# Optimization experiments

Hardware: AMD Instinct MI355X
Metric: run time of the kernel (lower is better)

## Reference

```python
import jax, jax.numpy as jnp
import numpy as np
from jax import lax

D_MODEL = 768
N_LAYER = 4
VOCAB = 50280  # 50277 padded to multiple of 8
D_INNER = 2 * D_MODEL
D_STATE = 16
D_CONV = 4
DT_RANK = 48  # ceil(768/16)
EPS = 1e-5


def setup_inputs() -> dict:
    key = jax.random.key(0)
    ks = iter(jax.random.split(key, 16))
    s = 0.02
    B, L = 1, 1024
    inp = {
        "input_ids": jax.random.randint(next(ks), (B, L), 0, 50277, dtype=jnp.int64).astype(jnp.int32),
        "embedding": jax.random.normal(next(ks), (VOCAB, D_MODEL), jnp.float32) * s,
        "in_proj_w": jax.random.normal(next(ks), (N_LAYER, 2 * D_INNER, D_MODEL), jnp.float32) * s,
        "conv_w": jax.random.normal(next(ks), (N_LAYER, D_INNER, 1, D_CONV), jnp.float32) * s,
        "conv_b": jnp.zeros((N_LAYER, D_INNER), jnp.float32),
        "x_proj_w": jax.random.normal(next(ks), (N_LAYER, DT_RANK + 2 * D_STATE, D_INNER), jnp.float32) * s,
        "dt_proj_w": jax.random.normal(next(ks), (N_LAYER, D_INNER, DT_RANK), jnp.float32) * s,
        "dt_proj_b": jax.random.uniform(next(ks), (N_LAYER, D_INNER), jnp.float32, -4.0, -2.0),
        "A_log": jnp.log(jnp.broadcast_to(jnp.arange(1, D_STATE + 1, dtype=jnp.float32), (N_LAYER, D_INNER, D_STATE))),
        "D_param": jnp.ones((N_LAYER, D_INNER), jnp.float32),
        "out_proj_w": jax.random.normal(next(ks), (N_LAYER, D_MODEL, D_INNER), jnp.float32) * s,
        "norm_w": jnp.ones((N_LAYER, D_MODEL), jnp.float32),
        "norm_f_w": jnp.ones((D_MODEL,), jnp.float32),
    }
    return inp


def rmsnorm(x, w):
    var = jnp.mean(jnp.square(x), axis=-1, keepdims=True)
    return x * lax.rsqrt(var + EPS) * w


def silu(x):
    return x * jax.nn.sigmoid(x)


def mamba_mixer(h, in_w, cw, cb, xw, dtw, dtb, A_log, Dp, ow):
    B, L, _ = h.shape
    xz = jnp.einsum("bld,ed->ble", h, in_w)          # [B,L,2*d_inner]
    x, z = jnp.split(xz, 2, axis=-1)
    # causal depthwise conv1d over length
    xc = lax.conv_general_dilated(
        x.transpose(0, 2, 1), cw, (1,), [(D_CONV - 1, 0)],
        dimension_numbers=("NCH", "OIH", "NCH"), feature_group_count=D_INNER,
    ).transpose(0, 2, 1) + cb                          # [B,L,d_inner]
    xc = silu(xc)
    dbl = jnp.einsum("bld,ed->ble", xc, xw)            # [B,L,R+2N]
    dt = jax.nn.softplus(jnp.einsum("blr,dr->bld", dbl[..., :DT_RANK], dtw) + dtb)
    Bm = dbl[..., DT_RANK:DT_RANK + D_STATE]           # [B,L,N]
    Cm = dbl[..., DT_RANK + D_STATE:]                  # [B,L,N]
    A = -jnp.exp(A_log)                                # [d_inner,N]
    dA = jnp.exp(dt[..., None] * A)                    # [B,L,d_inner,N]
    dBx = dt[..., None] * Bm[:, :, None, :] * xc[..., None]

    def step(s, inp):
        a, b, c = inp
        s = a * s + b
        y = jnp.einsum("bdn,bn->bd", s, c)
        return s, y

    s0 = jnp.zeros((B, D_INNER, D_STATE), h.dtype)
    _, ys = lax.scan(step, s0, (dA.transpose(1, 0, 2, 3), dBx.transpose(1, 0, 2, 3), Cm.transpose(1, 0, 2)))
    y = ys.transpose(1, 0, 2) + xc * Dp                # [B,L,d_inner]
    y = y * silu(z)
    return jnp.einsum("ble,de->bld", y, ow)


def reference(input_ids, embedding, in_proj_w, conv_w, conv_b, x_proj_w,
              dt_proj_w, dt_proj_b, A_log, D_param, out_proj_w, norm_w, norm_f_w):
    h = embedding[input_ids]                           # [B,L,D]
    for i in range(N_LAYER):
        h = h + mamba_mixer(rmsnorm(h, norm_w[i]), in_proj_w[i], conv_w[i], conv_b[i],
                            x_proj_w[i], dt_proj_w[i], dt_proj_b[i], A_log[i],
                            D_param[i], out_proj_w[i])
    h = rmsnorm(h, norm_f_w)
    logits = jnp.einsum("bld,vd->blv", h, embedding)   # tied lm_head
    return logits
```

## Files before the change

kernel.cpp:

```cpp
#include <hip/hip_runtime.h>
#include <cstdint>
#include <cstddef>

#define N_LAYER 4
#define VOCABSZ 50280
#define VOCABPAD 50304
#define DMODEL 768
#define DINNER 1536
#define DSTATE 16
#define DTRANK 48
#define SEQL 1024
#define HPSTRIDE (SEQL * DMODEL)

typedef __bf16 bf16x8 __attribute__((ext_vector_type(8)));
typedef unsigned short us8 __attribute__((ext_vector_type(8)));
typedef float f32x4 __attribute__((ext_vector_type(4)));

__device__ __forceinline__ unsigned short f2bf(float f) {
    unsigned int u = __builtin_bit_cast(unsigned int, f);
    u = (u + 0x7FFFu + ((u >> 16) & 1u)) >> 16;
    return (unsigned short)u;
}

__device__ __forceinline__ void glds16(const unsigned short* g, unsigned short* l) {
    __builtin_amdgcn_global_load_lds(
        (const __attribute__((address_space(1))) void*)g,
        (__attribute__((address_space(3))) void*)l, 16, 0, 0);
}

__device__ __forceinline__ void cvt8(const float* s, unsigned short* d) {
    const float4* s4 = (const float4*)s;
    float4 a = s4[0], b = s4[1];
    us8 o = { f2bf(a.x), f2bf(a.y), f2bf(a.z), f2bf(a.w),
              f2bf(b.x), f2bf(b.y), f2bf(b.z), f2bf(b.w) };
    *(us8*)d = o;
}

__global__ __launch_bounds__(256) void cvt_bf16_kernel(
    const float* __restrict__ src, unsigned short* __restrict__ dst, int n8)
{
    int i = blockIdx.x * 256 + threadIdx.x;
    if (i >= n8) return;
    cvt8(src + (size_t)i * 8, dst + (size_t)i * 8);
}

__global__ __launch_bounds__(256) void cvt3_kernel(
    const float* __restrict__ s0, unsigned short* __restrict__ d0, int n0,
    const float* __restrict__ s1, unsigned short* __restrict__ d1, int n1,
    const float* __restrict__ s2, unsigned short* __restrict__ d2, int n2)
{
    int i = blockIdx.x * 256 + threadIdx.x;
    const float* s; unsigned short* d; int j = i;
    if (j < n0) { s = s0; d = d0; }
    else {
        j -= n0;
        if (j < n1) { s = s1; d = d1; }
        else {
            j -= n1;
            if (j >= n2) return;
            s = s2; d = d2;
        }
    }
    cvt8(s + (size_t)j * 8, d + (size_t)j * 8);
}

__global__ __launch_bounds__(256) void cvt_xw_kernel(
    const float* __restrict__ xw, unsigned short* __restrict__ xwB)
{
    int g = blockIdx.x * 256 + threadIdx.x;
    if (g >= N_LAYER * 128 * 192) return;
    int row = g / 192;
    int c8  = g % 192;
    int layer = row >> 7;
    int r = row & 127;
    us8 o;
    if (r < 80) {
        const float4* s = (const float4*)(xw + ((size_t)(layer * 80 + r) * DINNER) + c8 * 8);
        float4 a = s[0], b = s[1];
        o = (us8){ f2bf(a.x), f2bf(a.y), f2bf(a.z), f2bf(a.w),
                   f2bf(b.x), f2bf(b.y), f2bf(b.z), f2bf(b.w) };
    } else {
        o = (us8){0, 0, 0, 0, 0, 0, 0, 0};
    }
    *(us8*)(xwB + (size_t)row * DINNER + c8 * 8) = o;
}

__device__ __forceinline__ void gemm_compute32(
    const unsigned short* sAbuf, const unsigned short* sBbuf,
    int wm, int wn, int frs, f32x4 (&acc)[4][4])
{
    bf16x8 af[4], bfr[4];
#pragma unroll
    for (int t = 0; t < 4; ++t) {
        af[t]  = __builtin_bit_cast(bf16x8, *(const us8*)&sAbuf[(wm + t * 16) * 32 + frs]);
        bfr[t] = __builtin_bit_cast(bf16x8, *(const us8*)&sBbuf[(wn + t * 16) * 32 + frs]);
    }
#pragma unroll
    for (int mt = 0; mt < 4; ++mt)
#pragma unroll
        for (int nt = 0; nt < 4; ++nt)
            acc[mt][nt] = __builtin_amdgcn_mfma_f32_16x16x32_bf16(
                af[mt], bfr[nt], acc[mt][nt], 0, 0, 0);
}

__device__ __forceinline__ void gemm_core(
    const unsigned short* __restrict__ A, const unsigned short* __restrict__ B,
    float* __restrict__ C, int N, int Kstride, int Klen, int bm, int bn)
{
    __shared__ unsigned short sA0[128 * 32];
    __shared__ unsigned short sA1[128 * 32];
    __shared__ unsigned short sB0[128 * 32];
    __shared__ unsigned short sB1[128 * 32];

    const int tid  = threadIdx.x;
    const int lane = tid & 63;
    const int wave = tid >> 6;
    const int wm = (wave & 1) * 64;
    const int wn = (wave >> 1) * 64;

    const int scol = ((tid & 3) ^ ((tid >> 3) & 3)) * 8;
    const unsigned short* Ag0 = A + (size_t)(bm + (tid >> 2)) * Kstride + scol;
    const unsigned short* Ag1 = Ag0 + (size_t)64 * Kstride;
    const unsigned short* Bg0 = B + (size_t)(bn + (tid >> 2)) * Kstride + scol;
    const unsigned short* Bg1 = Bg0 + (size_t)64 * Kstride;
    unsigned short* lA0a = sA0 + tid * 8;  unsigned short* lA0b = lA0a + 2048;
    unsigned short* lA1a = sA1 + tid * 8;  unsigned short* lA1b = lA1a + 2048;
    unsigned short* lB0a = sB0 + tid * 8;  unsigned short* lB0b = lB0a + 2048;
    unsigned short* lB1a = sB1 + tid * 8;  unsigned short* lB1b = lB1a + 2048;

    f32x4 acc[4][4];
#pragma unroll
    for (int i = 0; i < 4; ++i)
#pragma unroll
        for (int j = 0; j < 4; ++j) acc[i][j] = (f32x4){0.f, 0.f, 0.f, 0.f};

    const int frs = (lane & 15) * 32 + (((lane >> 4) ^ ((lane >> 1) & 3))) * 8;

    glds16(Ag0, lA0a); glds16(Ag1, lA0b);
    glds16(Bg0, lB0a); glds16(Bg1, lB0b);
    Ag0 += 32; Ag1 += 32; Bg0 += 32; Bg1 += 32;
    __syncthreads();

    for (int k0 = 0; k0 < Klen; k0 += 64) {
        glds16(Ag0, lA1a); glds16(Ag1, lA1b);
        glds16(Bg0, lB1a); glds16(Bg1, lB1b);
        Ag0 += 32; Ag1 += 32; Bg0 += 32; Bg1 += 32;
        gemm_compute32(sA0, sB0, wm, wn, frs, acc);
        __syncthreads();

        if (k0 + 64 < Klen) {
            glds16(Ag0, lA0a); glds16(Ag1, lA0b);
            glds16(Bg0, lB0a); glds16(Bg1, lB0b);
            Ag0 += 32; Ag1 += 32; Bg0 += 32; Bg1 += 32;
        }
        gemm_compute32(sA1, sB1, wm, wn, frs, acc);
        __syncthreads();
    }

    const int cn = lane & 15;
    const int cm = (lane >> 4) * 4;
#pragma unroll
    for (int mt = 0; mt < 4; ++mt) {
#pragma unroll
        for (int nt = 0; nt < 4; ++nt) {
            int n = bn + wn + nt * 16 + cn;
            if (n < N) {
#pragma unroll
                for (int r = 0; r < 4; ++r) {
                    int m = bm + wm + mt * 16 + cm + r;
                    C[(size_t)m * N + n] = acc[mt][nt][r];
                }
            }
        }
    }
}

__device__ __forceinline__ void swz_mn(int bid, int grid, int& bm, int& bn)
{
    int cpx = grid >> 3;
    int swz = (bid & 7) * cpx + (bid >> 3);
    bm = (swz & 7) << 7;
    bn = (swz >> 3) << 7;
}

__global__ __launch_bounds__(256) void gemm_in_kernel(
    const unsigned short* __restrict__ A, const unsigned short* __restrict__ B,
    float* __restrict__ C, int N, int K)
{ int bm, bn; swz_mn(blockIdx.x, gridDim.x, bm, bn); gemm_core(A, B, C, N, K, K, bm, bn); }

__global__ __launch_bounds__(256) void gemm_xproj_kernel(
    const unsigned short* __restrict__ A, const unsigned short* __restrict__ B,
    float* __restrict__ C, int N, int K)
{ int bm, bn; swz_mn(blockIdx.x, gridDim.x, bm, bn); gemm_core(A, B, C, N, K, K, bm, bn); }

__global__ __launch_bounds__(256) void gemm_logits_kernel(
    const unsigned short* __restrict__ A, const unsigned short* __restrict__ B,
    float* __restrict__ C, int N, int K)
{ int bm, bn; swz_mn(blockIdx.x, gridDim.x, bm, bn); gemm_core(A, B, C, N, K, K, bm, bn); }

__global__ __launch_bounds__(256) void gemm_outp_kernel(
    const unsigned short* __restrict__ A, const unsigned short* __restrict__ B,
    float* __restrict__ hp, int N, int Kstride, int Klen)
{
    int bid = blockIdx.x;
    int split = bid / 48;
    int r = bid - split * 48;
    int swz = (r & 7) * 6 + (r >> 3);
    int bm = (swz & 7) << 7;
    int bn = (swz >> 3) << 7;
    int kbase = split * Klen;
    gemm_core(A + kbase, B + kbase, hp + (size_t)split * HPSTRIDE,
              N, Kstride, Klen, bm, bn);
}

template <int ADD>
__global__ __launch_bounds__(256) void gemm_fb_kernel(
    const float* __restrict__ A, const float* __restrict__ B,
    const float* __restrict__ ADDSRC, float* __restrict__ C,
    int N, int K)
{
    __shared__ unsigned short sA[128 * 40];
    __shared__ unsigned short sB[128 * 40];
    const int tid  = threadIdx.x;
    const int lane = tid & 63;
    const int wave = tid >> 6;
    const int wm = (wave & 1) * 64;
    const int wn = (wave >> 1) * 64;
    const int bm = blockIdx.y * 128;
    const int bn = blockIdx.x * 128;
    const int srow = tid >> 1;
    const int scol = (tid & 1) * 16;
    const float* Ap = A + (size_t)(bm + srow) * K + scol;
    const int brow  = bn + srow;
    const bool bvalid = brow < N;
    const float* Bp = B + (size_t)(bvalid ? brow : 0) * K + scol;
    f32x4 acc[4][4];
#pragma unroll
    for (int i = 0; i < 4; ++i)
#pragma unroll
        for (int j = 0; j < 4; ++j) acc[i][j] = (f32x4){0.f, 0.f, 0.f, 0.f};
    unsigned short* sAp = &sA[srow * 40 + scol];
    unsigned short* sBp = &sB[srow * 40 + scol];
    const int fr = (lane & 15) * 40 + (lane >> 4) * 8;
    for (int k0 = 0; k0 < K; k0 += 32) {
        float4 a0 = *(const float4*)(Ap + k0);
        float4 a1 = *(const float4*)(Ap + k0 + 4);
        float4 a2 = *(const float4*)(Ap + k0 + 8);
        float4 a3 = *(const float4*)(Ap + k0 + 12);
        float4 b0, b1, b2, b3;
        if (bvalid) {
            b0 = *(const float4*)(Bp + k0);
            b1 = *(const float4*)(Bp + k0 + 4);
            b2 = *(const float4*)(Bp + k0 + 8);
            b3 = *(const float4*)(Bp + k0 + 12);
        } else {
            b0 = make_float4(0.f, 0.f, 0.f, 0.f);
            b1 = b0; b2 = b0; b3 = b0;
        }
        __syncthreads();
        us8 va0 = { f2bf(a0.x), f2bf(a0.y), f2bf(a0.z), f2bf(a0.w),
                    f2bf(a1.x), f2bf(a1.y), f2bf(a1.z), f2bf(a1.w) };
        us8 va1 = { f2bf(a2.x), f2bf(a2.y), f2bf(a2.z), f2bf(a2.w),
                    f2bf(a3.x), f2bf(a3.y), f2bf(a3.z), f2bf(a3.w) };
        us8 vb0 = { f2bf(b0.x), f2bf(b0.y), f2bf(b0.z), f2bf(b0.w),
                    f2bf(b1.x), f2bf(b1.y), f2bf(b1.z), f2bf(b1.w) };
        us8 vb1 = { f2bf(b2.x), f2bf(b2.y), f2bf(b2.z), f2bf(b2.w),
                    f2bf(b3.x), f2bf(b3.y), f2bf(b3.z), f2bf(b3.w) };
        *(us8*)(sAp)     = va0;
        *(us8*)(sAp + 8) = va1;
        *(us8*)(sBp)     = vb0;
        *(us8*)(sBp + 8) = vb1;
        __syncthreads();
        bf16x8 af[4], bfr[4];
#pragma unroll
        for (int t = 0; t < 4; ++t) {
            af[t]  = __builtin_bit_cast(bf16x8, *(const us8*)&sA[wm * 40 + t * 640 + fr]);
            bfr[t] = __builtin_bit_cast(bf16x8, *(const us8*)&sB[wn * 40 + t * 640 + fr]);
        }
#pragma unroll
        for (int mt = 0; mt < 4; ++mt)
#pragma unroll
            for (int nt = 0; nt < 4; ++nt)
                acc[mt][nt] = __builtin_amdgcn_mfma_f32_16x16x32_bf16(
                    af[mt], bfr[nt], acc[mt][nt], 0, 0, 0);
    }
    const int cn = lane & 15;
    const int cm = (lane >> 4) * 4;
#pragma unroll
    for (int mt = 0; mt < 4; ++mt) {
#pragma unroll
        for (int nt = 0; nt < 4; ++nt) {
            int n = bn + wn + nt * 16 + cn;
            if (n < N) {
#pragma unroll
                for (int r = 0; r < 4; ++r) {
                    int m = bm + wm + mt * 16 + cm + r;
                    size_t idx = (size_t)m * N + n;
                    float v = acc[mt][nt][r];
                    if constexpr (ADD) v += ADDSRC[idx];
                    C[idx] = v;
                }
            }
        }
    }
}

__global__ __launch_bounds__(256) void embed_kernel(
    const int* __restrict__ ids, const float* __restrict__ emb, float* __restrict__ h)
{
    int l = blockIdx.x;
    int id = ids[l];
    const float* src = emb + (size_t)id * DMODEL;
    for (int d = threadIdx.x; d < DMODEL; d += 256) h[(size_t)l * DMODEL + d] = src[d];
}

template <typename OT>
__global__ __launch_bounds__(256) void rmsnorm_kernel(
    const float* __restrict__ x, const float* __restrict__ w,
    OT* __restrict__ out, int D)
{
    int l = blockIdx.x;
    const float* xr = x + (size_t)l * D;
    float ss = 0.f;
    for (int d = threadIdx.x; d < D; d += 256) { float v = xr[d]; ss += v * v; }
#pragma unroll
    for (int off = 32; off > 0; off >>= 1) ss += __shfl_down(ss, off, 64);
    __shared__ float red[4];
    __shared__ float invs;
    if ((threadIdx.x & 63) == 0) red[threadIdx.x >> 6] = ss;
    __syncthreads();
    if (threadIdx.x == 0)
        invs = rsqrtf((red[0] + red[1] + red[2] + red[3]) / (float)D + 1e-5f);
    __syncthreads();
    float inv = invs;
    for (int d = threadIdx.x; d < D; d += 256) {
        float v = xr[d] * inv * w[d];
        if constexpr (sizeof(OT) == 2) out[(size_t)l * D + d] = f2bf(v);
        else                           out[(size_t)l * D + d] = v;
    }
}

__global__ __launch_bounds__(256) void rmsnorm_acc_kernel(
    float* __restrict__ h, const float* __restrict__ hp,
    const float* __restrict__ w, unsigned short* __restrict__ out)
{
    int l = blockIdx.x;
    const size_t base = (size_t)l * DMODEL;
    __shared__ float row[DMODEL];
    float ss = 0.f;
    for (int d = threadIdx.x; d < DMODEL; d += 256) {
        float v = h[base + d]
                + hp[base + d]
                + hp[base + d + (size_t)HPSTRIDE]
                + hp[base + d + (size_t)2 * HPSTRIDE]
                + hp[base + d + (size_t)3 * HPSTRIDE];
        row[d] = v;
        h[base + d] = v;
        ss += v * v;
    }
#pragma unroll
    for (int off = 32; off > 0; off >>= 1) ss += __shfl_down(ss, off, 64);
    __shared__ float red[4];
    __shared__ float invs;
    if ((threadIdx.x & 63) == 0) red[threadIdx.x >> 6] = ss;
    __syncthreads();
    if (threadIdx.x == 0)
        invs = rsqrtf((red[0] + red[1] + red[2] + red[3]) / (float)DMODEL + 1e-5f);
    __syncthreads();
    float inv = invs;
    for (int d = threadIdx.x; d < DMODEL; d += 256)
        out[base + d] = f2bf(row[d] * inv * w[d]);
}

__global__ __launch_bounds__(256) void conv_silu_kernel(
    const float* __restrict__ xz, const float* __restrict__ cw,
    const float* __restrict__ cb, float* __restrict__ xc,
    unsigned short* __restrict__ xcB)
{
    int l = blockIdx.x / 6;
    int d = (blockIdx.x % 6) * 256 + threadIdx.x;
    float w0 = cw[d * 4], w1 = cw[d * 4 + 1], w2 = cw[d * 4 + 2], w3 = cw[d * 4 + 3];
    float acc = cb[d];
    if (l >= 3) acc += xz[(size_t)(l - 3) * 3072 + d] * w0;
    if (l >= 2) acc += xz[(size_t)(l - 2) * 3072 + d] * w1;
    if (l >= 1) acc += xz[(size_t)(l - 1) * 3072 + d] * w2;
    acc += xz[(size_t)l * 3072 + d] * w3;
    float sig = 1.f / (1.f + __expf(-acc));
    float v = acc * sig;
    size_t idx = (size_t)l * DINNER + d;
    xc[idx]  = v;
    xcB[idx] = f2bf(v);
}

__global__ __launch_bounds__(256) void xproj_kernel(
    const float* __restrict__ xc, const float* __restrict__ xw, float* __restrict__ dbl)
{
    int l = blockIdx.x;
    __shared__ float sx[DINNER];
    for (int d = threadIdx.x; d < DINNER; d += 256) sx[d] = xc[(size_t)l * DINNER + d];
    __syncthreads();
    int wave = threadIdx.x >> 6, lane = threadIdx.x & 63;
    for (int e = wave * 20; e < wave * 20 + 20; ++e) {
        const float* wr = xw + (size_t)e * DINNER;
        float s = 0.f;
        for (int d = lane; d < DINNER; d += 64) s += sx[d] * wr[d];
#pragma unroll
        for (int off = 32; off > 0; off >>= 1) s += __shfl_down(s, off, 64);
        if (lane == 0) dbl[l * 80 + e] = s;
    }
}

__global__ __launch_bounds__(256) void dtproj_kernel(
    const float* __restrict__ dbl, const float* __restrict__ dtw,
    const float* __restrict__ dtb, float* __restrict__ dt)
{
    int l = blockIdx.x / 6;
    int e = (blockIdx.x % 6) * 256 + threadIdx.x;
    __shared__ float sd[48];
    if (threadIdx.x < 48) sd[threadIdx.x] = dbl[l * 80 + threadIdx.x];
    __syncthreads();
    float a = dtb[e];
    const float4* wr = (const float4*)(dtw + (size_t)e * 48);
#pragma unroll
    for (int q = 0; q < 12; ++q) {
        float4 w4 = wr[q];
        a += sd[q * 4] * w4.x + sd[q * 4 + 1] * w4.y + sd[q * 4 + 2] * w4.z + sd[q * 4 + 3] * w4.w;
    }
    dt[(size_t)l * DINNER + e] = (a > 20.f) ? a : log1pf(__expf(a));
}

template <typename OT>
__global__ __launch_bounds__(64) void scan_kernel(
    const float* __restrict__ dt, const float* __restrict__ dbl,
    const float* __restrict__ xc, const float* __restrict__ xz,
    const float* __restrict__ alog, const float* __restrict__ dpar,
    OT* __restrict__ yf)
{
    int d0 = blockIdx.x * 4;
    int lane = threadIdx.x;
    int n = lane & 15;
    int dloc = lane >> 4;
    int d = d0 + dloc;
    float A = -__expf(alog[d * 16 + n]);
    float Dq[4];
#pragma unroll
    for (int q = 0; q < 4; ++q) Dq[q] = dpar[d0 + q];

    __shared__ float sdt[64][4];
    __shared__ float sxc[64][4];
    __shared__ float sz[64][4];
    __shared__ float sB[64][16];
    __shared__ float sC[64][16];
    __shared__ float pp[4][64][17];

    float s = 0.f;
    for (int c0 = 0; c0 < SEQL; c0 += 64) {
        int l = c0 + lane;
        *(float4*)&sdt[lane][0] = *(const float4*)&dt[(size_t)l * DINNER + d0];
        *(float4*)&sxc[lane][0] = *(const float4*)&xc[(size_t)l * DINNER + d0];
        *(float4*)&sz[lane][0]  = *(const float4*)&xz[(size_t)l * 3072 + DINNER + d0];
#pragma unroll
        for (int q = 0; q < 4; ++q) {
            *(float4*)&sB[lane][q * 4] = *(const float4*)&dbl[l * 80 + 48 + q * 4];
            *(float4*)&sC[lane][q * 4] = *(const float4*)&dbl[l * 80 + 64 + q * 4];
        }
        __syncthreads();
#pragma unroll 4
        for (int j = 0; j < 64; ++j) {
            float dtv = sdt[j][dloc];
            float xv  = sxc[j][dloc];
            float a = __expf(dtv * A);
            s = fmaf(a, s, dtv * sB[j][n] * xv);
            pp[dloc][j][n] = s * sC[j][n];
        }
        __syncthreads();
#pragma unroll
        for (int q = 0; q < 4; ++q) {
            float accv = 0.f;
#pragma unroll
            for (int nn = 0; nn < 16; ++nn) accv += pp[q][lane][nn];
            float xv = sxc[lane][q];
            float zv = sz[lane][q];
            float sig = 1.f / (1.f + __expf(-zv));
            float v = (accv + xv * Dq[q]) * (zv * sig);
            if constexpr (sizeof(OT) == 2) yf[(size_t)(c0 + lane) * DINNER + d0 + q] = f2bf(v);
            else                           yf[(size_t)(c0 + lane) * DINNER + d0 + q] = v;
        }
        __syncthreads();
    }
}

__global__ __launch_bounds__(64) void scan_fused_kernel(
    const float* __restrict__ dbl, const float* __restrict__ xc,
    const float* __restrict__ xz, const float* __restrict__ dtw,
    const float* __restrict__ dtb, const float* __restrict__ alog,
    const float* __restrict__ dpar, unsigned short* __restrict__ yf)
{
    int d0 = blockIdx.x * 4;
    int lane = threadIdx.x;
    int n = lane & 15;
    int dloc = lane >> 4;
    int d = d0 + dloc;
    float A = -__expf(alog[d * 16 + n]);
    float Dq[4], dtbq[4];
#pragma unroll
    for (int q = 0; q < 4; ++q) { Dq[q] = dpar[d0 + q]; dtbq[q] = dtb[d0 + q]; }

    __shared__ float swt[4][48];
    for (int t = lane; t < 192; t += 64)
        swt[t / 48][t % 48] = dtw[(size_t)(d0 + t / 48) * 48 + t % 48];

    __shared__ float sdt[64][4];
    __shared__ float sxc[64][4];
    __shared__ float sz[64][4];
    __shared__ float sB[64][16];
    __shared__ float sC[64][16];
    __shared__ float pp[4][64][17];
    __syncthreads();

    float s = 0.f;
    for (int c0 = 0; c0 < SEQL; c0 += 64) {
        int l = c0 + lane;
        *(float4*)&sxc[lane][0] = *(const float4*)&xc[(size_t)l * DINNER + d0];
        *(float4*)&sz[lane][0]  = *(const float4*)&xz[(size_t)l * 3072 + DINNER + d0];
        float4 db[12];
#pragma unroll
        for (int q4 = 0; q4 < 12; ++q4)
            db[q4] = *(const float4*)&dbl[l * 80 + q4 * 4];
#pragma unroll
        for (int q = 0; q < 4; ++q) {
            *(float4*)&sB[lane][q * 4] = *(const float4*)&dbl[l * 80 + 48 + q * 4];
            *(float4*)&sC[lane][q * 4] = *(const float4*)&dbl[l * 80 + 64 + q * 4];
        }
#pragma unroll
        for (int q = 0; q < 4; ++q) {
            float a = dtbq[q];
#pragma unroll
            for (int q4 = 0; q4 < 12; ++q4) {
                float4 w4 = *(const float4*)&swt[q][q4 * 4];
                a += db[q4].x * w4.x + db[q4].y * w4.y + db[q4].z * w4.z + db[q4].w * w4.w;
            }
            sdt[lane][q] = (a > 20.f) ? a : log1pf(__expf(a));
        }
        __syncthreads();
#pragma unroll 4
        for (int j = 0; j < 64; ++j) {
            float dtv = sdt[j][dloc];
            float xv  = sxc[j][dloc];
            float a = __expf(dtv * A);
            s = fmaf(a, s, dtv * sB[j][n] * xv);
            pp[dloc][j][n] = s * sC[j][n];
        }
        __syncthreads();
#pragma unroll
        for (int q = 0; q < 4; ++q) {
            float accv = 0.f;
#pragma unroll
            for (int nn = 0; nn < 16; ++nn) accv += pp[q][lane][nn];
            float xv = sxc[lane][q];
            float zv = sz[lane][q];
            float sig = 1.f / (1.f + __expf(-zv));
            float v = (accv + xv * Dq[q]) * (zv * sig);
            yf[(size_t)(c0 + lane) * DINNER + d0 + q] = f2bf(v);
        }
        __syncthreads();
    }
}

extern "C" void kernel_launch(void* const* d_in, const int* in_sizes, int n_in,
                              void* d_out, int out_size, void* d_ws, size_t ws_size,
                              hipStream_t stream)
{
    const int*   ids  = (const int*)d_in[0];
    const float* emb  = (const float*)d_in[1];
    const float* inw  = (const float*)d_in[2];
    const float* cw   = (const float*)d_in[3];
    const float* cb   = (const float*)d_in[4];
    const float* xw   = (const float*)d_in[5];
    const float* dtw  = (const float*)d_in[6];
    const float* dtb  = (const float*)d_in[7];
    const float* alog = (const float*)d_in[8];
    const float* dpar = (const float*)d_in[9];
    const float* ow   = (const float*)d_in[10];
    const float* nw   = (const float*)d_in[11];
    const float* nfw  = (const float*)d_in[12];
    float* out = (float*)d_out;

    const size_t MAIN_WS = 138936320ull;

    if (ws_size >= MAIN_WS) {
        char* p = (char*)d_ws;
        float* h    = (float*)p;                 p += (size_t)SEQL * DMODEL * 4;
        float* xz   = (float*)p;                 p += (size_t)SEQL * 3072 * 4;
        float* xc   = (float*)p;                 p += (size_t)SEQL * DINNER * 4;
        float* dbl  = (float*)p;                 p += (size_t)SEQL * 80 * 4;
        float* dt_unused = (float*)p;            p += (size_t)SEQL * DINNER * 4;
        unsigned short* xnB  = (unsigned short*)p; p += (size_t)SEQL * DMODEL * 2;
        unsigned short* yfB  = (unsigned short*)p; p += (size_t)SEQL * DINNER * 2;
        unsigned short* embB = (unsigned short*)p; p += (size_t)VOCABPAD * DMODEL * 2;
        unsigned short* inwB = (unsigned short*)p; p += (size_t)N_LAYER * 3072 * DMODEL * 2;
        unsigned short* owB  = (unsigned short*)p; p += (size_t)N_LAYER * DMODEL * DINNER * 2;
        (void)dt_unused;

        unsigned short* xwB = (unsigned short*)out;
        unsigned short* xcB = xwB + (size_t)N_LAYER * 128 * DINNER;
        float* hp = (float*)(xcB + (size_t)SEQL * DINNER);

        const int n0 = VOCABSZ * DMODEL / 8;
        const int n1 = N_LAYER * 3072 * DMODEL / 8;
        const int n2 = N_LAYER * DMODEL * DINNER / 8;
        cvt3_kernel<<<(n0 + n1 + n2 + 255) / 256, 256, 0, stream>>>(
            emb, embB, n0, inw, inwB, n1, ow, owB, n2);
        cvt_xw_kernel<<<(N_LAYER * 128 * 192 + 255) / 256, 256, 0, stream>>>(xw, xwB);

        embed_kernel<<<SEQL, 256, 0, stream>>>(ids, emb, h);

        for (int i = 0; i < N_LAYER; ++i) {
            if (i == 0)
                rmsnorm_kernel<unsigned short><<<SEQL, 256, 0, stream>>>(
                    h, nw, xnB, DMODEL);
            else
                rmsnorm_acc_kernel<<<SEQL, 256, 0, stream>>>(
                    h, hp, nw + (size_t)i * DMODEL, xnB);
            gemm_in_kernel<<<8 * (3072 / 128), 256, 0, stream>>>(
                xnB, inwB + (size_t)i * 3072 * DMODEL, xz, 3072, DMODEL);
            conv_silu_kernel<<<SEQL * 6, 256, 0, stream>>>(
                xz, cw + (size_t)i * DINNER * 4, cb + (size_t)i * DINNER, xc, xcB);
            gemm_xproj_kernel<<<8, 256, 0, stream>>>(
                xcB, xwB + (size_t)i * 128 * DINNER, dbl, 80, DINNER);
            scan_fused_kernel<<<DINNER / 4, 64, 0, stream>>>(
                dbl, xc, xz, dtw + (size_t)i * DINNER * DTRANK,
                dtb + (size_t)i * DINNER, alog + (size_t)i * DINNER * DSTATE,
                dpar + (size_t)i * DINNER, yfB);
            gemm_outp_kernel<<<4 * 48, 256, 0, stream>>>(
                yfB, owB + (size_t)i * DMODEL * DINNER, hp, DMODEL, DINNER, DINNER / 4);
        }

        rmsnorm_acc_kernel<<<SEQL, 256, 0, stream>>>(h, hp, nfw, xnB);
        gemm_logits_kernel<<<8 * ((VOCABSZ + 127) / 128), 256, 0, stream>>>(
            xnB, embB, out, VOCABSZ, DMODEL);
    } else {
        float* h   = (float*)d_ws;
        float* xn  = h  + (size_t)SEQL * DMODEL;
        float* xz  = xn + (size_t)SEQL * DMODEL;
        float* xc  = xz + (size_t)SEQL * 3072;
        float* dbl = xc + (size_t)SEQL * DINNER;
        float* dt  = dbl + (size_t)SEQL * 80;
        float* yf  = dt + (size_t)SEQL * DINNER;
        unsigned short* xcB = (unsigned short*)out;

        embed_kernel<<<SEQL, 256, 0, stream>>>(ids, emb, h);
        for (int i = 0; i < N_LAYER; ++i) {
            rmsnorm_kernel<float><<<SEQL, 256, 0, stream>>>(h, nw + (size_t)i * DMODEL, xn, DMODEL);
            gemm_fb_kernel<0><<<dim3(3072 / 128, SEQL / 128), 256, 0, stream>>>(
                xn, inw + (size_t)i * 3072 * DMODEL, nullptr, xz, 3072, DMODEL);
            conv_silu_kernel<<<SEQL * 6, 256, 0, stream>>>(
                xz, cw + (size_t)i * DINNER * 4, cb + (size_t)i * DINNER, xc, xcB);
            xproj_kernel<<<SEQL, 256, 0, stream>>>(xc, xw + (size_t)i * 80 * DINNER, dbl);
            dtproj_kernel<<<SEQL * 6, 256, 0, stream>>>(
                dbl, dtw + (size_t)i * DINNER * DTRANK, dtb + (size_t)i * DINNER, dt);
            scan_kernel<float><<<DINNER / 4, 64, 0, stream>>>(
                dt, dbl, xc, xz, alog + (size_t)i * DINNER * DSTATE, dpar + (size_t)i * DINNER, yf);
            gemm_fb_kernel<1><<<dim3(DMODEL / 128, SEQL / 128), 256, 0, stream>>>(
                yf, ow + (size_t)i * DMODEL * DINNER, h, h, DMODEL, DINNER);
        }
        rmsnorm_kernel<float><<<SEQL, 256, 0, stream>>>(h, nfw, xn, DMODEL);
        gemm_fb_kernel<0><<<dim3((VOCABSZ + 127) / 128, SEQL / 128), 256, 0, stream>>>(
            xn, emb, nullptr, out, VOCABSZ, DMODEL);
    }
}
```

Measured before the change: 1.199 ms.

## Split-K x_proj GEMM, prefetch scan chunks, and specialize logits GEMM

The x_proj GEMM, which ran on only 8 blocks, is split along K into 8 partial products over 64 blocks, followed by a small reduction kernel, so more of the GPU is busy. The scan kernel now loads the next 64-step chunk into registers while the current chunk is being processed, hiding global load latency, and keeps x and z in registers instead of rereading shared memory. The logits GEMM gets a dedicated kernel with no K-split and a bounds check on N. The costs are an extra launch, partial-sum buffer traffic, and higher register pressure in the scan.

```diff
diff --git a/kernel.cpp b/kernel.cpp
--- a/kernel.cpp
+++ b/kernel.cpp
@@ -11,6 +11,7 @@
 #define DTRANK 48
 #define SEQL 1024
 #define HPSTRIDE (SEQL * DMODEL)
+#define XPSTRIDE (SEQL * 80)
 
 typedef __bf16 bf16x8 __attribute__((ext_vector_type(8)));
 typedef unsigned short us8 __attribute__((ext_vector_type(8)));
@@ -188,15 +189,28 @@
     float* __restrict__ C, int N, int K)
 { int bm, bn; swz_mn(blockIdx.x, gridDim.x, bm, bn); gemm_core(A, B, C, N, K, K, bm, bn); }
 
-__global__ __launch_bounds__(256) void gemm_xproj_kernel(
+__global__ __launch_bounds__(256) void gemm_xprojk_kernel(
     const unsigned short* __restrict__ A, const unsigned short* __restrict__ B,
-    float* __restrict__ C, int N, int K)
-{ int bm, bn; swz_mn(blockIdx.x, gridDim.x, bm, bn); gemm_core(A, B, C, N, K, K, bm, bn); }
-
-__global__ __launch_bounds__(256) void gemm_logits_kernel(
-    const unsigned short* __restrict__ A, const unsigned short* __restrict__ B,
-    float* __restrict__ C, int N, int K)
-{ int bm, bn; swz_mn(blockIdx.x, gridDim.x, bm, bn); gemm_core(A, B, C, N, K, K, bm, bn); }
+    float* __restrict__ xpp)
+{
+    int split = blockIdx.x >> 3;
+    int bm = (blockIdx.x & 7) << 7;
+    int kbase = split * 192;
+    gemm_core(A + kbase, B + kbase, xpp + (size_t)split * XPSTRIDE,
+              80, DINNER, 192, bm, 0);
+}
+
+__global__ __launch_bounds__(256) void xred_kernel(
+    const float* __restrict__ xpp, float* __restrict__ dbl)
+{
+    int i = blockIdx.x * 256 + threadIdx.x;
+    if (i >= XPSTRIDE / 4) return;
+    const f32x4* p = (const f32x4*)xpp + i;
+    f32x4 s = p[0];
+#pragma unroll
+    for (int k = 1; k < 8; ++k) s += p[(size_t)k * (XPSTRIDE / 4)];
+    ((f32x4*)dbl)[i] = s;
+}
 
 __global__ __launch_bounds__(256) void gemm_outp_kernel(
     const unsigned short* __restrict__ A, const unsigned short* __restrict__ B,
@@ -211,6 +225,68 @@
     int kbase = split * Klen;
     gemm_core(A + kbase, B + kbase, hp + (size_t)split * HPSTRIDE,
               N, Kstride, Klen, bm, bn);
+}
+
+__global__ __launch_bounds__(256) void gemm_logits_kernel(
+    const unsigned short* __restrict__ A, const unsigned short* __restrict__ B,
+    float* __restrict__ C, int N, int K)
+{
+    __shared__ unsigned short sA[128 * 32];
+    __shared__ unsigned short sB[128 * 32];
+
+    const int tid  = threadIdx.x;
+    const int lane = tid & 63;
+    const int wave = tid >> 6;
+    const int wm = (wave & 1) * 64;
+    const int wn = (wave >> 1) * 64;
+    int bm, bn;
+    swz_mn(blockIdx.x, gridDim.x, bm, bn);
+
+    const int scol = ((tid & 3) ^ ((tid >> 3) & 3)) * 8;
+    const unsigned short* Ag0 = A + (size_t)(bm + (tid >> 2)) * K + scol;
+    const unsigned short* Ag1 = Ag0 + (size_t)64 * K;
+    const unsigned short* Bg0 = B + (size_t)(bn + (tid >> 2)) * K + scol;
+    const unsigned short* Bg1 = Bg0 + (size_t)64 * K;
+    unsigned short* lA0 = sA + tid * 8;
+    unsigned short* lA1 = lA0 + 2048;
+    unsigned short* lB0 = sB + tid * 8;
+    unsigned short* lB1 = lB0 + 2048;
+
+    f32x4 acc[4][4];
+#pragma unroll
+    for (int i = 0; i < 4; ++i)
+#pragma unroll
+        for (int j = 0; j < 4; ++j) acc[i][j] = (f32x4){0.f, 0.f, 0.f, 0.f};
+
+    const int frs = (lane & 15) * 32 + (((lane >> 4) ^ ((lane >> 1) & 3))) * 8;
+
+    for (int k0 = 0; k0 < K; k0 += 32) {
+        __syncthreads();
+        glds16(Ag0, lA0);
+        glds16(Ag1, lA1);
+        glds16(Bg0, lB0);
+        glds16(Bg1, lB1);
+        Ag0 += 32; Ag1 += 32; Bg0 += 32; Bg1 += 32;
+        __syncthreads();
+        gemm_compute32(sA, sB, wm, wn, frs, acc);
+    }
+
+    const int cn = lane & 15;
+    const int cm = (lane >> 4) * 4;
+#pragma unroll
+    for (int mt = 0; mt < 4; ++mt) {
+#pragma unroll
+        for (int nt = 0; nt < 4; ++nt) {
+            int n = bn + wn + nt * 16 + cn;
+            if (n < N) {
+#pragma unroll
+                for (int r = 0; r < 4; ++r) {
+                    int m = bm + wm + mt * 16 + cm + r;
+                    C[(size_t)m * N + n] = acc[mt][nt][r];
+                }
+            }
+        }
+    }
 }
 
 template <int ADD>
@@ -516,21 +592,34 @@
     __shared__ float sB[64][16];
     __shared__ float sC[64][16];
     __shared__ float pp[4][64][17];
+
+    float4 rxc, rz, rdb[12], rB[4], rC[4];
+
+    auto loadchunk = [&](int c0) {
+        int l = c0 + lane;
+        rxc = *(const float4*)&xc[(size_t)l * DINNER + d0];
+        rz  = *(const float4*)&xz[(size_t)l * 3072 + DINNER + d0];
+#pragma unroll
+        for (int q4 = 0; q4 < 12; ++q4)
+            rdb[q4] = *(const float4*)&dbl[l * 80 + q4 * 4];
+#pragma unroll
+        for (int q = 0; q < 4; ++q) {
+            rB[q] = *(const float4*)&dbl[l * 80 + 48 + q * 4];
+            rC[q] = *(const float4*)&dbl[l * 80 + 64 + q * 4];
+        }
+    };
+
+    loadchunk(0);
     __syncthreads();
 
     float s = 0.f;
     for (int c0 = 0; c0 < SEQL; c0 += 64) {
-        int l = c0 + lane;
-        *(float4*)&sxc[lane][0] = *(const float4*)&xc[(size_t)l * DINNER + d0];
-        *(float4*)&sz[lane][0]  = *(const float4*)&xz[(size_t)l * 3072 + DINNER + d0];
-        float4 db[12];
-#pragma unroll
-        for (int q4 = 0; q4 < 12; ++q4)
-            db[q4] = *(const float4*)&dbl[l * 80 + q4 * 4];
+        *(float4*)&sxc[lane][0] = rxc;
+        *(float4*)&sz[lane][0]  = rz;
 #pragma unroll
         for (int q = 0; q < 4; ++q) {
-            *(float4*)&sB[lane][q * 4] = *(const float4*)&dbl[l * 80 + 48 + q * 4];
-            *(float4*)&sC[lane][q * 4] = *(const float4*)&dbl[l * 80 + 64 + q * 4];
+            *(float4*)&sB[lane][q * 4] = rB[q];
+            *(float4*)&sC[lane][q * 4] = rC[q];
         }
 #pragma unroll
         for (int q = 0; q < 4; ++q) {
@@ -538,11 +627,16 @@
 #pragma unroll
             for (int q4 = 0; q4 < 12; ++q4) {
                 float4 w4 = *(const float4*)&swt[q][q4 * 4];
-                a += db[q4].x * w4.x + db[q4].y * w4.y + db[q4].z * w4.z + db[q4].w * w4.w;
+                a += rdb[q4].x * w4.x + rdb[q4].y * w4.y + rdb[q4].z * w4.z + rdb[q4].w * w4.w;
             }
             sdt[lane][q] = (a > 20.f) ? a : log1pf(__expf(a));
         }
-        __syncthreads();
+        float excv[4] = { rxc.x, rxc.y, rxc.z, rxc.w };
+        float ezv[4]  = { rz.x,  rz.y,  rz.z,  rz.w  };
+        __syncthreads();
+
+        if (c0 + 64 < SEQL) loadchunk(c0 + 64);
+
 #pragma unroll 4
         for (int j = 0; j < 64; ++j) {
             float dtv = sdt[j][dloc];
@@ -557,10 +651,9 @@
             float accv = 0.f;
 #pragma unroll
             for (int nn = 0; nn < 16; ++nn) accv += pp[q][lane][nn];
-            float xv = sxc[lane][q];
-            float zv = sz[lane][q];
+            float zv = ezv[q];
             float sig = 1.f / (1.f + __expf(-zv));
-            float v = (accv + xv * Dq[q]) * (zv * sig);
+            float v = (accv + excv[q] * Dq[q]) * (zv * sig);
             yf[(size_t)(c0 + lane) * DINNER + d0 + q] = f2bf(v);
         }
         __syncthreads();
@@ -604,7 +697,8 @@
 
         unsigned short* xwB = (unsigned short*)out;
         unsigned short* xcB = xwB + (size_t)N_LAYER * 128 * DINNER;
-        float* hp = (float*)(xcB + (size_t)SEQL * DINNER);
+        float* hp  = (float*)(xcB + (size_t)SEQL * DINNER);
+        float* xpp = hp + (size_t)4 * HPSTRIDE;
 
         const int n0 = VOCABSZ * DMODEL / 8;
         const int n1 = N_LAYER * 3072 * DMODEL / 8;
@@ -626,8 +720,9 @@
                 xnB, inwB + (size_t)i * 3072 * DMODEL, xz, 3072, DMODEL);
             conv_silu_kernel<<<SEQL * 6, 256, 0, stream>>>(
                 xz, cw + (size_t)i * DINNER * 4, cb + (size_t)i * DINNER, xc, xcB);
-            gemm_xproj_kernel<<<8, 256, 0, stream>>>(
-                xcB, xwB + (size_t)i * 128 * DINNER, dbl, 80, DINNER);
+            gemm_xprojk_kernel<<<64, 256, 0, stream>>>(
+                xcB, xwB + (size_t)i * 128 * DINNER, xpp);
+            xred_kernel<<<(XPSTRIDE / 4 + 255) / 256, 256, 0, stream>>>(xpp, dbl);
             scan_fused_kernel<<<DINNER / 4, 64, 0, stream>>>(
                 dbl, xc, xz, dtw + (size_t)i * DINNER * DTRANK,
                 dtb + (size_t)i * DINNER, alog + (size_t)i * DINNER * DSTATE,
```

Measured after the change: 1.105 ms. 1.08x faster.
